# Optimization experiments

Measured on AMD Instinct MI355X. Metric: run time of the kernel, lower is better.

Reference implementation:

```python
import jax, jax.numpy as jnp
import numpy as np

B, Hg, Wg, DIM, HEADS, WS, SHIFT = 16, 64, 64, 512, 16, 8, 4
HIDDEN = 4 * DIM
PRIOR_BETA = 1.0
EPS = 1e-5


def _layernorm(x, g, b):
    m = jnp.mean(x, axis=-1, keepdims=True)
    v = jnp.mean(jnp.square(x - m), axis=-1, keepdims=True)
    return (x - m) / jnp.sqrt(v + EPS) * g + b


def _rel_pos_index(ws):
    coords = np.stack(np.meshgrid(np.arange(ws), np.arange(ws), indexing='ij')).reshape(2, -1)
    rel = (coords[:, :, None] - coords[:, None, :]).transpose(1, 2, 0)
    rel[..., 0] += ws - 1
    rel[..., 1] += ws - 1
    rel[..., 0] *= 2 * ws - 1
    return rel.sum(-1)  # (N, N) int


def _shift_mask(H, W, ws, shift):
    img = np.zeros((H, W))
    cnt = 0
    for hs in (slice(0, -ws), slice(-ws, -shift), slice(-shift, None)):
        for wsl in (slice(0, -ws), slice(-ws, -shift), slice(-shift, None)):
            img[hs, wsl] = cnt
            cnt += 1
    N = ws * ws
    mw = img.reshape(H // ws, ws, W // ws, ws).transpose(0, 2, 1, 3).reshape(-1, N)
    am = mw[:, None, :] - mw[:, :, None]
    return np.where(am != 0, -100.0, 0.0).astype(np.float32)  # (nW, N, N)


def setup_inputs() -> dict:
    key = jax.random.key(0)
    ks = jax.random.split(key, 8)
    s = 0.02
    return {
        'x': jax.random.normal(ks[0], (B, Hg * Wg, DIM), jnp.float32),
        'M_map': jax.random.uniform(ks[1], (B, Hg, Wg, 1), jnp.float32),
        'norm1_g': jnp.ones((DIM,), jnp.float32),
        'norm1_b': jnp.zeros((DIM,), jnp.float32),
        'qkv_w': jax.random.normal(ks[2], (3 * DIM, DIM), jnp.float32) * s,
        'qkv_b': jnp.zeros((3 * DIM,), jnp.float32),
        'proj_w': jax.random.normal(ks[3], (DIM, DIM), jnp.float32) * s,
        'proj_b': jnp.zeros((DIM,), jnp.float32),
        'rpb_table': jax.random.normal(ks[4], ((2 * WS - 1) ** 2, HEADS), jnp.float32) * s,
        'norm2_g': jnp.ones((DIM,), jnp.float32),
        'norm2_b': jnp.zeros((DIM,), jnp.float32),
        'fc1_w': jax.random.normal(ks[5], (HIDDEN, DIM), jnp.float32) * s,
        'fc1_b': jnp.zeros((HIDDEN,), jnp.float32),
        'fc2_w': jax.random.normal(ks[6], (DIM, HIDDEN), jnp.float32) * s,
        'fc2_b': jnp.zeros((DIM,), jnp.float32),
        'H': Hg,
        'W': Wg,
    }


def reference(x, M_map, norm1_g, norm1_b, qkv_w, qkv_b, proj_w, proj_b, rpb_table,
              norm2_g, norm2_b, fc1_w, fc1_b, fc2_w, fc2_b, H, W):
    Bsz, L, C = x.shape
    ws, shift, heads = WS, SHIFT, HEADS
    N = ws * ws
    hd = C // heads
    scale = hd ** -0.5

    shortcut = x
    y = _layernorm(x, norm1_g, norm1_b).reshape(Bsz, H, W, C)
    Mm = jnp.clip(M_map[..., 0], 0.0, 1.0)  # (B, H, W)

    # cyclic shift (SW-MSA)
    y = jnp.roll(y, (-shift, -shift), axis=(1, 2))
    Mm = jnp.roll(Mm, (-shift, -shift), axis=(1, 2))

    # window partition -> (B*nW, N, C) and (B*nW, N)
    def win_part(t):
        c = t.shape[-1]
        t = t.reshape(Bsz, H // ws, ws, W // ws, ws, c)
        return t.transpose(0, 1, 3, 2, 4, 5).reshape(-1, N, c)

    xw = win_part(y)
    mw = win_part(Mm[..., None])[..., 0]
    B_ = xw.shape[0]

    qkv = (xw @ qkv_w.T + qkv_b).reshape(B_, N, 3, heads, hd).transpose(2, 0, 3, 1, 4)
    q, k, v = qkv[0], qkv[1], qkv[2]  # each (B_, heads, N, hd)
    attn = jnp.einsum('bhnd,bhmd->bhnm', q * scale, k)

    # relative position bias (heads, N, N)
    rpi = _rel_pos_index(ws)
    rpb = rpb_table[rpi.reshape(-1)].reshape(N, N, heads).transpose(2, 0, 1)
    attn = attn + rpb[None]

    # semantic prior bias: 0.5*(M_i + M_j), broadcast over heads
    sb = 0.5 * (mw[:, :, None] + mw[:, None, :])  # (B_, N, N)
    attn = attn + PRIOR_BETA * sb[:, None]

    # shift mask
    am = jnp.asarray(_shift_mask(H, W, ws, shift), attn.dtype)  # (nW, N, N)
    nW = am.shape[0]
    attn = attn.reshape(Bsz, nW, heads, N, N) + am[None, :, None]
    attn = attn.reshape(B_, heads, N, N)

    attn = jax.nn.softmax(attn, axis=-1)
    out = jnp.einsum('bhnm,bhmd->bhnd', attn, v).transpose(0, 2, 1, 3).reshape(B_, N, C)
    out = out @ proj_w.T + proj_b

    # window reverse + reverse shift
    out = out.reshape(Bsz, H // ws, W // ws, ws, ws, C).transpose(0, 1, 3, 2, 4, 5).reshape(Bsz, H, W, C)
    out = jnp.roll(out, (shift, shift), axis=(1, 2)).reshape(Bsz, L, C)

    x1 = shortcut + out
    h = jax.nn.gelu(_layernorm(x1, norm2_g, norm2_b) @ fc1_w.T + fc1_b, approximate=False)
    return x1 + (h @ fc2_w.T + fc2_b)
```

## Files before the change

### kernel.cpp

```cpp
#include <hip/hip_runtime.h>
#include <hip/hip_bf16.h>

typedef unsigned short u16;
typedef unsigned int u32;
typedef __attribute__((ext_vector_type(4))) float f32x4;
typedef __attribute__((ext_vector_type(8))) short bf16x8;

#define DEV static __device__ __forceinline__

DEV float bf2f(u16 u) { u32 x = ((u32)u) << 16; return __builtin_bit_cast(float, x); }
DEV u16 f2bf(float f) {
  __hip_bfloat16 h = __float2bfloat16(f);
  return __builtin_bit_cast(u16, h);
}

DEV void gld16(const u16* g, u16* l) {
  __builtin_amdgcn_global_load_lds((const __attribute__((address_space(1))) void*)g,
                                   (__attribute__((address_space(3))) void*)l, 16, 0, 0);
}

__global__ void cvt_bf16(const float* __restrict__ s, u16* __restrict__ d, int n) {
  int i = blockIdx.x * 256 + threadIdx.x;
  if (i < n) d[i] = f2bf(s[i]);
}

__global__ __launch_bounds__(256)
void ln_bf16(const float* __restrict__ src, const float* __restrict__ g,
             const float* __restrict__ b, u16* __restrict__ dst) {
  const int row = blockIdx.x * 4 + (threadIdx.x >> 6);
  const int lane = threadIdx.x & 63;
  const float* p = src + (long)row * 512 + lane * 8;
  float x[8];
  *(float4*)&x[0] = *(const float4*)p;
  *(float4*)&x[4] = *(const float4*)(p + 4);
  float s = 0.f;
#pragma unroll
  for (int e = 0; e < 8; ++e) s += x[e];
#pragma unroll
  for (int off = 32; off; off >>= 1) s += __shfl_xor(s, off, 64);
  const float mean = s * (1.0f / 512.0f);
  float q = 0.f;
#pragma unroll
  for (int e = 0; e < 8; ++e) { float d = x[e] - mean; q += d * d; }
#pragma unroll
  for (int off = 32; off; off >>= 1) q += __shfl_xor(q, off, 64);
  const float rinv = rsqrtf(q * (1.0f / 512.0f) + 1e-5f);
  u16 o[8];
  const int c0 = lane * 8;
#pragma unroll
  for (int e = 0; e < 8; ++e) o[e] = f2bf((x[e] - mean) * rinv * g[c0 + e] + b[c0 + e]);
  *(uint4*)(dst + (long)row * 512 + c0) = *(uint4*)o;
}

enum { EPI_QKV = 0, EPI_PROJ = 1, EPI_GELU = 2, EPI_FC2 = 3 };

template <int EPI>
__global__ __launch_bounds__(512, 2)
void gemm256(const u16* __restrict__ A, const u16* __restrict__ W,
             const float* __restrict__ bias, const float* __restrict__ res,
             void* __restrict__ outv, int M, int N, int K) {
  extern __shared__ u16 sm[];
  (void)M;
  const int t = threadIdx.x;
  const int lane = t & 63;
  const int wave = t >> 6;
  const int wm = wave >> 2;
  const int wn = wave & 3;
  const long m0 = (long)blockIdx.y * 256;
  const long n0 = (long)blockIdx.x * 256;

  const int sr = t >> 2;
  const int sc = ((t & 3) ^ ((sr >> 1) & 3)) * 8;
  const u16* gA0 = A + (m0 + sr) * (long)K + sc;
  const u16* gA1 = gA0 + 128L * K;
  const u16* gB0 = W + (n0 + sr) * (long)K + sc;
  const u16* gB1 = gB0 + 128L * K;
  u16* lws = sm + wave * 512;

  const int NT = K >> 5;
  f32x4 acc[8][4] = {};
  const int fr = lane & 15;
  const int kp = ((lane >> 4) ^ ((fr >> 1) & 3)) * 8;

#define STAGE(slot, tile)                      \
  do {                                         \
    const int _k = (tile) * 32;                \
    u16* _b = lws + (slot) * 16384;            \
    gld16(gA0 + _k, _b);                       \
    gld16(gA1 + _k, _b + 4096);                \
    gld16(gB0 + _k, _b + 8192);                \
    gld16(gB1 + _k, _b + 12288);               \
  } while (0)

#define COMPUTE(slot)                                                                           \
  do {                                                                                          \
    const u16* Ab = sm + (slot) * 16384 + (wm * 128 + fr) * 32 + kp;                            \
    const u16* Bb = sm + (slot) * 16384 + 8192 + (wn * 64 + fr) * 32 + kp;                      \
    bf16x8 af[8], bfv[4];                                                                       \
    _Pragma("unroll")                                                                           \
    for (int i = 0; i < 8; ++i) af[i] = *(const bf16x8*)(Ab + i * 512);                         \
    _Pragma("unroll")                                                                           \
    for (int j = 0; j < 4; ++j) bfv[j] = *(const bf16x8*)(Bb + j * 512);                        \
    __builtin_amdgcn_s_setprio(1);                                                              \
    _Pragma("unroll")                                                                           \
    for (int i = 0; i < 8; ++i)                                                                 \
      _Pragma("unroll")                                                                         \
      for (int j = 0; j < 4; ++j)                                                               \
        acc[i][j] = __builtin_amdgcn_mfma_f32_16x16x32_bf16(af[i], bfv[j], acc[i][j], 0, 0, 0); \
    __builtin_amdgcn_s_setprio(0);                                                              \
  } while (0)

  STAGE(0, 0);
  STAGE(1, 1);
  STAGE(2, 2);
  asm volatile("s_waitcnt vmcnt(8)" ::: "memory");
  __builtin_amdgcn_s_barrier();
  asm volatile("" ::: "memory");

  int kt = 0;
  for (; kt < NT - 3; ++kt) {
    STAGE((kt + 3) & 3, kt + 3);
    COMPUTE(kt & 3);
    asm volatile("s_waitcnt vmcnt(8)" ::: "memory");
    __builtin_amdgcn_s_barrier();
    asm volatile("" ::: "memory");
  }
  COMPUTE(kt & 3);
  asm volatile("s_waitcnt vmcnt(4)" ::: "memory");
  __builtin_amdgcn_s_barrier();
  asm volatile("" ::: "memory");
  ++kt;
  COMPUTE(kt & 3);
  asm volatile("s_waitcnt vmcnt(0)" ::: "memory");
  __builtin_amdgcn_s_barrier();
  asm volatile("" ::: "memory");
  ++kt;
  COMPUTE(kt & 3);
#undef STAGE
#undef COMPUTE

  const int col = lane & 15;
  const int rq = (lane >> 4) * 4;
#pragma unroll
  for (int mi = 0; mi < 8; ++mi) {
#pragma unroll
    for (int ni = 0; ni < 4; ++ni) {
#pragma unroll
      for (int r = 0; r < 4; ++r) {
        const long m = m0 + wm * 128 + mi * 16 + rq + r;
        const long n = n0 + wn * 64 + ni * 16 + col;
        const float v = acc[mi][ni][r] + bias[n];
        const long idx = m * (long)N + n;
        if constexpr (EPI == EPI_QKV) {
          ((u16*)outv)[idx] = f2bf(v);
        } else if constexpr (EPI == EPI_PROJ) {
          ((float*)outv)[idx] = v + res[idx];
        } else if constexpr (EPI == EPI_GELU) {
          ((u16*)outv)[idx] = f2bf(0.5f * v * (1.0f + erff(v * 0.70710678118f)));
        } else {
          ((float*)outv)[idx] = v + res[idx];
        }
      }
    }
  }
}

constexpr int SS_S = 68;
constexpr int VT_S = 72;

__global__ __launch_bounds__(256)
void attn_mfma(const u16* __restrict__ qkv, const float* __restrict__ mmap,
               const float* __restrict__ rpb, u16* __restrict__ outp) {
  __shared__ u16 SSb[4 * 64 * SS_S];
  __shared__ u16 Vtb[4 * 32 * VT_S];
  __shared__ u16 rpb_s[16 * 226];
  __shared__ float mw[64];
  __shared__ int tok[64];
  __shared__ int regi[64];

  const int t = threadIdx.x;
  const int lane = t & 63, wave = t >> 6;
  const int c = lane & 15, q = lane >> 4;
  const int win = blockIdx.x;
  const int b = win >> 6, wh = (win >> 3) & 7, ww = win & 7;

  if (t < 64) {
    const int i = t >> 3, j = t & 7;
    const int hs = wh * 8 + i, wsv = ww * 8 + j;
    const int h = (hs + 4) & 63, w = (wsv + 4) & 63;
    const int tk = b * 4096 + h * 64 + w;
    tok[t] = tk;
    mw[t] = fminf(fmaxf(mmap[tk], 0.f), 1.f);
    regi[t] = (hs < 56 ? 0 : (hs < 60 ? 1 : 2)) * 3 + (wsv < 56 ? 0 : (wsv < 60 ? 1 : 2));
  }
  for (int id = t; id < 3600; id += 256) {
    const int h = id & 15, idx = id >> 4;
    rpb_s[h * 226 + idx] = f2bf(rpb[id]);
  }
  __syncthreads();

  u16* SS = SSb + wave * 64 * SS_S;
  u16* Vt = Vtb + wave * 32 * VT_S;

  int tQ[4];
  float mwn[16], mwm[4];
  int rgn[16], rgm[4];
#pragma unroll
  for (int i = 0; i < 4; ++i) tQ[i] = tok[16 * i + c];
#pragma unroll
  for (int i = 0; i < 4; ++i)
#pragma unroll
    for (int r = 0; r < 4; ++r) {
      const int n = 16 * i + 4 * q + r;
      mwn[i * 4 + r] = mw[n];
      rgn[i * 4 + r] = regi[n];
    }
#pragma unroll
  for (int j = 0; j < 4; ++j) {
    const int m = 16 * j + c;
    mwm[j] = mw[m];
    rgm[j] = regi[m];
  }
  const int imc = c >> 3, jmc = c & 7;
  const int tV = tok[lane];
  const float scale = 0.17677669529663687f;

  for (int hi = 0; hi < 4; ++hi) {
    const int head = wave * 4 + hi;

    bf16x8 qf[4], kf[4];
#pragma unroll
    for (int i = 0; i < 4; ++i) {
      const u16* base = qkv + (long)tQ[i] * 1536 + head * 32 + q * 8;
      qf[i] = *(const bf16x8*)(base);
      kf[i] = *(const bf16x8*)(base + 512);
    }

    {
      const u16* vp = qkv + (long)tV * 1536 + 1024 + head * 32;
      u16 vv[32];
      *(uint4*)&vv[0]  = *(const uint4*)(vp);
      *(uint4*)&vv[8]  = *(const uint4*)(vp + 8);
      *(uint4*)&vv[16] = *(const uint4*)(vp + 16);
      *(uint4*)&vv[24] = *(const uint4*)(vp + 24);
#pragma unroll
      for (int d = 0; d < 32; ++d) Vt[d * VT_S + lane] = vv[d];
    }

    f32x4 acc[4][4] = {};
#pragma unroll
    for (int i = 0; i < 4; ++i)
#pragma unroll
      for (int j = 0; j < 4; ++j)
        acc[i][j] = __builtin_amdgcn_mfma_f32_16x16x32_bf16(qf[i], kf[j], acc[i][j], 0, 0, 0);

    const u16* rb = rpb_s + head * 226;
    float rmx[16], rsum[16];
#pragma unroll
    for (int i = 0; i < 4; ++i)
#pragma unroll
      for (int r = 0; r < 4; ++r) {
        const int n = 16 * i + 4 * q + r;
        const int inr = n >> 3, jnr = n & 7;
        float mx = -1e30f;
#pragma unroll
        for (int j = 0; j < 4; ++j) {
          const int di = inr - 2 * j - imc + 7;
          const int dj = jnr - jmc + 7;
          float s = acc[i][j][r] * scale + bf2f(rb[di * 15 + dj]) +
                    0.5f * (mwn[i * 4 + r] + mwm[j]);
          if (rgn[i * 4 + r] != rgm[j]) s -= 100.f;
          acc[i][j][r] = s;
          mx = fmaxf(mx, s);
        }
        rmx[i * 4 + r] = mx;
      }
#pragma unroll
    for (int ir = 0; ir < 16; ++ir)
#pragma unroll
      for (int msk = 1; msk < 16; msk <<= 1)
        rmx[ir] = fmaxf(rmx[ir], __shfl_xor(rmx[ir], msk, 64));
#pragma unroll
    for (int i = 0; i < 4; ++i)
#pragma unroll
      for (int r = 0; r < 4; ++r) {
        float sm = 0.f;
#pragma unroll
        for (int j = 0; j < 4; ++j) {
          const float e = __expf(acc[i][j][r] - rmx[i * 4 + r]);
          acc[i][j][r] = e;
          sm += e;
        }
        rsum[i * 4 + r] = sm;
      }
#pragma unroll
    for (int ir = 0; ir < 16; ++ir) {
#pragma unroll
      for (int msk = 1; msk < 16; msk <<= 1)
        rsum[ir] += __shfl_xor(rsum[ir], msk, 64);
      rsum[ir] = 1.0f / rsum[ir];
    }

#pragma unroll
    for (int i = 0; i < 4; ++i)
#pragma unroll
      for (int j = 0; j < 4; ++j) {
        ushort4 pk;
        pk.x = f2bf(acc[i][j][0] * rsum[i * 4 + 0]);
        pk.y = f2bf(acc[i][j][1] * rsum[i * 4 + 1]);
        pk.z = f2bf(acc[i][j][2] * rsum[i * 4 + 2]);
        pk.w = f2bf(acc[i][j][3] * rsum[i * 4 + 3]);
        *(ushort4*)&SS[(16 * j + c) * SS_S + 16 * i + 4 * q] = pk;
      }

    __syncthreads();

    bf16x8 av[2][2];
#pragma unroll
    for (int mi = 0; mi < 2; ++mi)
#pragma unroll
      for (int ki = 0; ki < 2; ++ki)
        av[mi][ki] = *(const bf16x8*)&Vt[(16 * mi + c) * VT_S + 32 * ki + 8 * q];

    f32x4 oacc[2][4] = {};
#pragma unroll
    for (int ki = 0; ki < 2; ++ki)
#pragma unroll
      for (int ni = 0; ni < 4; ++ni) {
        union { u16 h[8]; bf16x8 v; } ub;
#pragma unroll
        for (int jj = 0; jj < 8; ++jj)
          ub.h[jj] = SS[(32 * ki + 8 * q + jj) * SS_S + 16 * ni + c];
#pragma unroll
        for (int mi = 0; mi < 2; ++mi)
          oacc[mi][ni] = __builtin_amdgcn_mfma_f32_16x16x32_bf16(av[mi][ki], ub.v, oacc[mi][ni], 0, 0, 0);
      }

#pragma unroll
    for (int ni = 0; ni < 4; ++ni) {
      u16* ob = outp + (long)tQ[ni] * 512 + head * 32;
#pragma unroll
      for (int mi = 0; mi < 2; ++mi) {
        ushort4 pk;
        pk.x = f2bf(oacc[mi][ni][0]);
        pk.y = f2bf(oacc[mi][ni][1]);
        pk.z = f2bf(oacc[mi][ni][2]);
        pk.w = f2bf(oacc[mi][ni][3]);
        *(ushort4*)(ob + 16 * mi + 4 * q) = pk;
      }
    }
    __syncthreads();
  }
}

extern "C" void kernel_launch(void* const* d_in, const int* in_sizes, int n_in,
                              void* d_out, int out_size, void* d_ws, size_t ws_size,
                              hipStream_t stream) {
  (void)in_sizes; (void)n_in; (void)out_size; (void)ws_size;
  const float* x      = (const float*)d_in[0];
  const float* mmap   = (const float*)d_in[1];
  const float* n1g    = (const float*)d_in[2];
  const float* n1b    = (const float*)d_in[3];
  const float* qkv_w  = (const float*)d_in[4];
  const float* qkv_b  = (const float*)d_in[5];
  const float* proj_w = (const float*)d_in[6];
  const float* proj_b = (const float*)d_in[7];
  const float* rpb    = (const float*)d_in[8];
  const float* n2g    = (const float*)d_in[9];
  const float* n2b    = (const float*)d_in[10];
  const float* fc1_w  = (const float*)d_in[11];
  const float* fc1_b  = (const float*)d_in[12];
  const float* fc2_w  = (const float*)d_in[13];
  const float* fc2_b  = (const float*)d_in[14];
  float* out = (float*)d_out;
  char* ws = (char*)d_ws;

  u16*   ybf   = (u16*)(ws);
  u16*   qkvbf = (u16*)(ws + (64L  << 20));
  u16*   attno = (u16*)(ws + (256L << 20));
  float* x1    = (float*)(ws + (320L << 20));
  u16*   hbuf  = qkvbf;
  u16*   wqkv  = (u16*)(ws + (448L << 20));
  u16*   wproj = wqkv + 1536 * 512;
  u16*   wfc1  = wproj + 512 * 512;
  u16*   wfc2  = wfc1 + 2048 * 512;

  static bool smem_init = false;
  if (!smem_init) {
    smem_init = true;
    (void)hipFuncSetAttribute(reinterpret_cast<const void*>(gemm256<EPI_QKV>),
                              hipFuncAttributeMaxDynamicSharedMemorySize, 131072);
    (void)hipFuncSetAttribute(reinterpret_cast<const void*>(gemm256<EPI_PROJ>),
                              hipFuncAttributeMaxDynamicSharedMemorySize, 131072);
    (void)hipFuncSetAttribute(reinterpret_cast<const void*>(gemm256<EPI_GELU>),
                              hipFuncAttributeMaxDynamicSharedMemorySize, 131072);
    (void)hipFuncSetAttribute(reinterpret_cast<const void*>(gemm256<EPI_FC2>),
                              hipFuncAttributeMaxDynamicSharedMemorySize, 131072);
  }

  cvt_bf16<<<1536 * 512 / 256, 256, 0, stream>>>(qkv_w, wqkv, 1536 * 512);
  cvt_bf16<<<512 * 512 / 256, 256, 0, stream>>>(proj_w, wproj, 512 * 512);
  cvt_bf16<<<2048 * 512 / 256, 256, 0, stream>>>(fc1_w, wfc1, 2048 * 512);
  cvt_bf16<<<512 * 2048 / 256, 256, 0, stream>>>(fc2_w, wfc2, 512 * 2048);

  ln_bf16<<<16384, 256, 0, stream>>>(x, n1g, n1b, ybf);
  gemm256<EPI_QKV><<<dim3(6, 256), 512, 131072, stream>>>(ybf, wqkv, qkv_b, nullptr, qkvbf, 65536, 1536, 512);
  attn_mfma<<<1024, 256, 0, stream>>>(qkvbf, mmap, rpb, attno);
  gemm256<EPI_PROJ><<<dim3(2, 256), 512, 131072, stream>>>(attno, wproj, proj_b, x, x1, 65536, 512, 512);
  ln_bf16<<<16384, 256, 0, stream>>>(x1, n2g, n2b, ybf);
  gemm256<EPI_GELU><<<dim3(8, 256), 512, 131072, stream>>>(ybf, wfc1, fc1_b, nullptr, hbuf, 65536, 2048, 512);
  gemm256<EPI_FC2><<<dim3(2, 256), 512, 131072, stream>>>(hbuf, wfc2, fc2_b, x1, out, 65536, 512, 2048);
}
```

Before: 1.062 ms.

## Split GEMM k-step into two half-phases interleaving staging with MFMA clusters

```diff
diff --git a/kernel.cpp b/kernel.cpp
--- a/kernel.cpp
+++ b/kernel.cpp
@@ -82,62 +82,88 @@
   const int fr = lane & 15;
   const int kp = ((lane >> 4) ^ ((fr >> 1) & 3)) * 8;
 
-#define STAGE(slot, tile)                      \
+#define STAGE_A(slot, tile)                    \
   do {                                         \
     const int _k = (tile) * 32;                \
     u16* _b = lws + (slot) * 16384;            \
     gld16(gA0 + _k, _b);                       \
     gld16(gA1 + _k, _b + 4096);                \
+  } while (0)
+
+#define STAGE_B(slot, tile)                    \
+  do {                                         \
+    const int _k = (tile) * 32;                \
+    u16* _b = lws + (slot) * 16384;            \
     gld16(gB0 + _k, _b + 8192);                \
     gld16(gB1 + _k, _b + 12288);               \
   } while (0)
 
-#define COMPUTE(slot)                                                                           \
-  do {                                                                                          \
-    const u16* Ab = sm + (slot) * 16384 + (wm * 128 + fr) * 32 + kp;                            \
-    const u16* Bb = sm + (slot) * 16384 + 8192 + (wn * 64 + fr) * 32 + kp;                      \
-    bf16x8 af[8], bfv[4];                                                                       \
-    _Pragma("unroll")                                                                           \
-    for (int i = 0; i < 8; ++i) af[i] = *(const bf16x8*)(Ab + i * 512);                         \
-    _Pragma("unroll")                                                                           \
-    for (int j = 0; j < 4; ++j) bfv[j] = *(const bf16x8*)(Bb + j * 512);                        \
-    __builtin_amdgcn_s_setprio(1);                                                              \
-    _Pragma("unroll")                                                                           \
-    for (int i = 0; i < 8; ++i)                                                                 \
-      _Pragma("unroll")                                                                         \
-      for (int j = 0; j < 4; ++j)                                                               \
-        acc[i][j] = __builtin_amdgcn_mfma_f32_16x16x32_bf16(af[i], bfv[j], acc[i][j], 0, 0, 0); \
-    __builtin_amdgcn_s_setprio(0);                                                              \
+#define COMPUTE2(slot, SA, SB)                                                                   \
+  do {                                                                                           \
+    const u16* Ab = sm + (slot) * 16384 + (wm * 128 + fr) * 32;                                  \
+    const u16* Bb = sm + (slot) * 16384 + 8192 + (wn * 64 + fr) * 32;                            \
+    bf16x8 af[4], bfv[4];                                                                        \
+    _Pragma("unroll")                                                                            \
+    for (int i = 0; i < 4; ++i) af[i] = *(const bf16x8*)(Ab + i * 512 + kp);                     \
+    _Pragma("unroll")                                                                            \
+    for (int j = 0; j < 4; ++j) bfv[j] = *(const bf16x8*)(Bb + j * 512 + kp);                    \
+    SA;                                                                                          \
+    __builtin_amdgcn_s_barrier();                                                                \
+    asm volatile("s_waitcnt lgkmcnt(0)" ::: "memory");                                           \
+    __builtin_amdgcn_sched_barrier(0);                                                           \
+    __builtin_amdgcn_s_setprio(1);                                                               \
+    _Pragma("unroll")                                                                            \
+    for (int i = 0; i < 4; ++i)                                                                  \
+      _Pragma("unroll")                                                                          \
+      for (int j = 0; j < 4; ++j)                                                                \
+        acc[i][j] = __builtin_amdgcn_mfma_f32_16x16x32_bf16(af[i], bfv[j], acc[i][j], 0, 0, 0);  \
+    __builtin_amdgcn_s_setprio(0);                                                               \
+    __builtin_amdgcn_s_barrier();                                                                \
+    bf16x8 ag[4];                                                                                \
+    _Pragma("unroll")                                                                            \
+    for (int i = 0; i < 4; ++i) ag[i] = *(const bf16x8*)(Ab + (4 + i) * 512 + kp);               \
+    SB;                                                                                          \
+    __builtin_amdgcn_s_barrier();                                                                \
+    asm volatile("s_waitcnt lgkmcnt(0)" ::: "memory");                                           \
+    __builtin_amdgcn_sched_barrier(0);                                                           \
+    __builtin_amdgcn_s_setprio(1);                                                               \
+    _Pragma("unroll")                                                                            \
+    for (int i = 0; i < 4; ++i)                                                                  \
+      _Pragma("unroll")                                                                          \
+      for (int j = 0; j < 4; ++j)                                                                \
+        acc[4 + i][j] =                                                                          \
+            __builtin_amdgcn_mfma_f32_16x16x32_bf16(ag[i], bfv[j], acc[4 + i][j], 0, 0, 0);      \
+    __builtin_amdgcn_s_setprio(0);                                                               \
   } while (0)
 
-  STAGE(0, 0);
-  STAGE(1, 1);
-  STAGE(2, 2);
+  STAGE_A(0, 0); STAGE_B(0, 0);
+  STAGE_A(1, 1); STAGE_B(1, 1);
+  STAGE_A(2, 2); STAGE_B(2, 2);
   asm volatile("s_waitcnt vmcnt(8)" ::: "memory");
   __builtin_amdgcn_s_barrier();
   asm volatile("" ::: "memory");
 
   int kt = 0;
   for (; kt < NT - 3; ++kt) {
-    STAGE((kt + 3) & 3, kt + 3);
-    COMPUTE(kt & 3);
+    COMPUTE2(kt & 3, STAGE_A((kt + 3) & 3, kt + 3), STAGE_B((kt + 3) & 3, kt + 3));
     asm volatile("s_waitcnt vmcnt(8)" ::: "memory");
     __builtin_amdgcn_s_barrier();
     asm volatile("" ::: "memory");
   }
-  COMPUTE(kt & 3);
+  COMPUTE2(kt & 3, (void)0, (void)0);
   asm volatile("s_waitcnt vmcnt(4)" ::: "memory");
   __builtin_amdgcn_s_barrier();
   asm volatile("" ::: "memory");
   ++kt;
-  COMPUTE(kt & 3);
+  COMPUTE2(kt & 3, (void)0, (void)0);
   asm volatile("s_waitcnt vmcnt(0)" ::: "memory");
   __builtin_amdgcn_s_barrier();
   asm volatile("" ::: "memory");
   ++kt;
-  COMPUTE(kt & 3);
-#undef STAGE
-#undef COMPUTE
+  COMPUTE2(kt & 3, (void)0, (void)0);
+#undef STAGE_A
+#undef STAGE_B
+#undef COMPUTE2
 
   const int col = lane & 15;
   const int rq = (lane >> 4) * 4;
```

Measured after the change: 1.081 ms. No clear change (+1.8%).
